# Optimization experiments

Hardware: AMD Instinct MI355X
Metric: run time of the kernel (lower is better)

The kernel has to match this reference:

```python
import jax, jax.numpy as jnp
import numpy as np

B, S, C = 16, 1024, 8
V, D, E, H, R = 50257, 512, 8, 512, 32
F, RT, CD, Q = 1024, 512, 64, 128
EPS = 1e-6


def _normalize(x):
    n = jnp.maximum(jnp.linalg.norm(x, axis=-1, keepdims=True), EPS)
    return x / n


def _fake_quantize(x):
    # F.normalize then straight-through int8 quant on the unit vector
    xn = _normalize(x)
    q = jnp.clip(jnp.round(xn * 127.0), -127.0, 127.0)
    return xn + jax.lax.stop_gradient(q / 127.0 - xn)


def setup_inputs() -> dict:
    key = jax.random.key(0)
    ks = iter(jax.random.split(key, 64))

    def w(shape, s=0.02):
        return (jax.random.normal(next(ks), shape, dtype=jnp.float32) * s)

    inp = {}
    inp['prefix_tokens'] = jax.random.randint(next(ks), (B, S), 0, V, dtype=jnp.int32)
    inp['chunk_inputs'] = jax.random.randint(next(ks), (B, C), 0, V, dtype=jnp.int32)
    inp['chunk_targets'] = jax.random.randint(next(ks), (B, C), 0, V, dtype=jnp.int32)
    inp['next_chunk_tokens'] = jax.random.randint(next(ks), (B, C), 0, V, dtype=jnp.int32)

    inp['emb'] = w((V, D))
    # stacked per-expert AffineExpert params
    inp['Wa'] = w((E, D, H)); inp['ba'] = jnp.zeros((E, H), jnp.float32)
    inp['Wg'] = w((E, D, R)); inp['bg'] = jnp.zeros((E, R), jnp.float32)
    inp['Wu'] = w((E, D, H)); inp['bu'] = jnp.zeros((E, H), jnp.float32)
    inp['u_mat'] = w((E, H, R)); inp['v_mat'] = w((E, H, R))
    inp['Wp'] = w((E, H, F)); inp['bp'] = jnp.zeros((E, F), jnp.float32)
    # gate MLP
    inp['Wg1'] = w((D, D)); inp['bg1'] = jnp.zeros((D,), jnp.float32)
    inp['Wg2'] = w((D, E)); inp['bg2'] = jnp.zeros((E,), jnp.float32)
    # query / target / key / code-expansion / write-code
    inp['Wq'] = w((F, Q)); inp['bq'] = jnp.zeros((Q,), jnp.float32)
    inp['Wt1'] = w((2 * D, RT)); inp['bt1'] = jnp.zeros((RT,), jnp.float32)
    inp['Wt2'] = w((RT, RT)); inp['bt2'] = jnp.zeros((RT,), jnp.float32)
    inp['Wk'] = w((RT, Q)); inp['bk'] = jnp.zeros((Q,), jnp.float32)
    inp['Web'] = w((CD, RT))  # expansion_basis (no bias)
    inp['Wwc'] = w((F, CD)); inp['bwc'] = jnp.zeros((CD,), jnp.float32)
    # ctx MLP
    inp['Wc1'] = w((2 * F, F)); inp['bc1'] = jnp.zeros((F,), jnp.float32)
    inp['Wc2'] = w((F, F)); inp['bc2'] = jnp.zeros((F,), jnp.float32)
    # chunk decoder
    inp['chunk_pos'] = w((C, F))
    inp['Wci'] = w((D + F, F)); inp['bci'] = jnp.zeros((F,), jnp.float32)
    inp['Wm1'] = w((F, F)); inp['bm1'] = jnp.zeros((F,), jnp.float32)
    inp['Wm2'] = w((F, F)); inp['bm2'] = jnp.zeros((F,), jnp.float32)
    inp['Wlm'] = w((F, V)); inp['blm'] = jnp.zeros((V,), jnp.float32)
    return inp


def _expert_scan(x, Wa, ba, Wg, bg, Wu, bu, u_mat, v_mat):
    # x: [B,S,D]; precompute all per-step projections as one big GEMM each,
    # leading axis = time for lax.scan. A,U: [S,E,B,H], G: [S,E,B,R]
    A = jax.nn.sigmoid(jnp.einsum('bsd,edh->sebh', x, Wa) + ba[None, :, None, :])
    G = jnp.einsum('bsd,edr->sebr', x, Wg) + bg[None, :, None, :]
    U = jnp.einsum('bsd,edh->sebh', x, Wu) + bu[None, :, None, :]

    def step(state, inp):  # state: [E,B,H]
        a, g, u = inp
        low = jnp.einsum('ebh,ehr->ebr', state, v_mat) * g
        state = a * state + u + jnp.einsum('ebr,ehr->ebh', low, u_mat)
        return state, None

    state0 = jnp.zeros((E, B, H), x.dtype)
    state, _ = jax.lax.scan(step, state0, (A, G, U))
    return state  # [E,B,H]


def reference(prefix_tokens, chunk_inputs, chunk_targets, next_chunk_tokens,
              emb, Wa, ba, Wg, bg, Wu, bu, u_mat, v_mat, Wp, bp,
              Wg1, bg1, Wg2, bg2, Wq, bq, Wt1, bt1, Wt2, bt2, Wk, bk,
              Web, Wwc, bwc, Wc1, bc1, Wc2, bc2,
              chunk_pos, Wci, bci, Wm1, bm1, Wm2, bm2, Wlm, blm):
    # ---- encode_prefix ----
    prefix_emb = emb[prefix_tokens]                       # [B,S,D]
    summary = prefix_emb.mean(axis=1)                     # [B,D]
    gate_probs = jax.nn.softmax(jax.nn.silu(summary @ Wg1 + bg1) @ Wg2 + bg2, axis=-1)  # [B,E]
    states = _expert_scan(prefix_emb, Wa, ba, Wg, bg, Wu, bu, u_mat, v_mat)             # [E,B,H]
    proj = jnp.einsum('ebh,ehf->ebf', states, Wp) + bp[:, None, :]                       # [E,B,F]
    fused = jnp.einsum('ebf,be->bf', proj, gate_probs)    # [B,F]

    # ---- query / target / key ----
    q_st = _fake_quantize(fused @ Wq + bq)                # [B,Q]
    chunk_emb = emb[chunk_targets].mean(axis=1)           # [B,D]
    next_emb = emb[next_chunk_tokens].mean(axis=1)        # [B,D]
    t_in = jnp.concatenate([chunk_emb, next_emb], axis=-1)
    target_state = _normalize(jax.nn.silu(t_in @ Wt1 + bt1) @ Wt2 + bt2)  # [B,RT]
    target_k_st = _fake_quantize(target_state @ Wk + bk)  # [B,Q]

    # ---- read_context (bank=None path -> zero read) ----
    zero_read = jnp.zeros_like(fused)
    c_in = jnp.concatenate([fused, zero_read], axis=-1)
    ctx = jax.nn.silu(c_in @ Wc1 + bc1) @ Wc2 + bc2       # [B,F]

    # ---- write_from_ctx ----
    write_codes = ctx @ Wwc + bwc                         # [B,CD]
    write_state = _normalize(write_codes @ Web)           # [B,RT]
    write_k_st = _fake_quantize(write_state @ Wk + bk)    # [B,Q]

    # ---- decode_chunk ----
    tok = emb[chunk_inputs]                               # [B,C,D]
    ctx_rep = jnp.broadcast_to(ctx[:, None, :], (B, C, F))
    hidden = jnp.concatenate([tok, ctx_rep], axis=-1) @ Wci + bci + chunk_pos[None]  # [B,C,F]
    hidden = jax.nn.silu(hidden @ Wm1 + bm1) @ Wm2 + bm2
    logits = hidden @ Wlm + blm                           # [B,C,V]

    # ---- losses ----
    logp = jax.nn.log_softmax(logits, axis=-1)
    token_loss = -jnp.take_along_axis(logp, chunk_targets[..., None], axis=-1)[..., 0]
    loss_nll = token_loss.mean()
    sim = (q_st @ target_k_st.T) / jnp.sqrt(jnp.float32(Q))  # [B,B]
    return logits, loss_nll, sim, write_k_st
```

## Files before the change

kernel.cpp:

```cpp
#include <hip/hip_runtime.h>
#include <math.h>

constexpr int BB = 16;
constexpr int SS = 1024;
constexpr int CC = 8;
constexpr int VV = 50257;
constexpr int DD = 512;
constexpr int EE = 8;
constexpr int HH = 512;
constexpr int RR = 32;
constexpr int FF = 1024;
constexpr int RTd = 512;
constexpr int CDd = 64;
constexpr int QQ = 128;
constexpr int SCH = 128;

typedef short bf16x8 __attribute__((ext_vector_type(8)));
typedef float f32x4 __attribute__((ext_vector_type(4)));

__device__ __forceinline__ float sigm(float x){ return 1.0f/(1.0f+expf(-x)); }

__device__ __forceinline__ unsigned short f2bf(float f){
  unsigned int u = __float_as_uint(f);
  u += 0x7fff + ((u>>16)&1);
  return (unsigned short)(u>>16);
}
__device__ __forceinline__ float bf2f(unsigned short h){
  return __uint_as_float(((unsigned int)h)<<16);
}

__device__ __forceinline__ void gload16(unsigned short* l, const unsigned short* g){
  __builtin_amdgcn_global_load_lds(
      (const __attribute__((address_space(1))) unsigned int*)(g),
      (__attribute__((address_space(3))) unsigned int*)(l), 16, 0, 0);
}

__global__ __launch_bounds__(256) void gather_pack(const int* __restrict__ toks,
    const float* __restrict__ emb, unsigned short* __restrict__ xp){
  int id = blockIdx.x*256 + threadIdx.x;
  int b = id >> 17;
  int rem = id & 131071;
  int c = rem >> 14;
  int rem2 = rem & 16383;
  int kc = rem2 >> 10;
  int pb = rem2 & 1023;
  int row = pb >> 3, q = pb & 7;
  int v = q ^ (row & 7);
  int kq = v >> 1, h = v & 1;
  int tok = toks[b*SS + c*128 + row];
  const float* src = emb + (size_t)tok*DD + kc*32 + kq*8;
  unsigned short o[8];
  #pragma unroll
  for (int j=0;j<8;j++){
    float f = src[j];
    unsigned short hi = f2bf(f);
    o[j] = h ? f2bf(f - bf2f(hi)) : hi;
  }
  ushort4* dst = (ushort4*)(xp + (size_t)id*8);
  dst[0] = make_ushort4(o[0],o[1],o[2],o[3]);
  dst[1] = make_ushort4(o[4],o[5],o[6],o[7]);
}

__global__ __launch_bounds__(512) void colsum_part(const int* __restrict__ toks,
    const float* __restrict__ emb, float* __restrict__ part){
  int b = blockIdx.y, j = blockIdx.x, d = threadIdx.x;
  float s = 0.f;
  for (int k=0;k<64;k++){
    int tok = toks[b*SS + j*64 + k];
    s += emb[(size_t)tok*DD + d];
  }
  part[(b*16 + j)*DD + d] = s;
}
__global__ __launch_bounds__(512) void colsum_final(const float* __restrict__ part,
                                                    float* __restrict__ summary){
  int b = blockIdx.x, d = threadIdx.x;
  float s = 0.f;
  for (int j=0;j<16;j++) s += part[(b*16 + j)*DD + d];
  summary[b*DD + d] = s * (1.0f/1024.0f);
}

__global__ __launch_bounds__(128) void gate_h1(const float* __restrict__ summary,
                                               const float* __restrict__ Wg1,
                                               const float* __restrict__ bg1,
                                               float* __restrict__ h1){
  int t = threadIdx.x; int j = blockIdx.x*128 + t;
  __shared__ float sm[16*512];
  for (int idx=t; idx<8192; idx+=128) sm[idx] = summary[idx];
  __syncthreads();
  float acc[16] = {0};
  for (int d=0; d<DD; d++){
    float w = Wg1[d*DD + j];
    #pragma unroll
    for (int b2=0;b2<16;b2++) acc[b2] += sm[b2*DD + d]*w;
  }
  #pragma unroll
  for (int b2=0;b2<16;b2++){ float v = acc[b2] + bg1[j]; h1[b2*DD + j] = v*sigm(v); }
}
__global__ __launch_bounds__(128) void gate_probs_k(const float* __restrict__ h1,
                                                    const float* __restrict__ Wg2,
                                                    const float* __restrict__ bg2,
                                                    float* __restrict__ gate){
  int t = threadIdx.x;
  int b = t>>3, e = t&7;
  float acc = bg2[e];
  for (int d=0; d<DD; d++) acc += h1[b*DD + d]*Wg2[d*EE + e];
  __shared__ float lg[16][8];
  lg[b][e] = acc;
  __syncthreads();
  if (e==0){
    float m = -3.4e38f;
    for (int i=0;i<8;i++) m = fmaxf(m, lg[b][i]);
    float s = 0.f; float ex[8];
    for (int i=0;i<8;i++){ ex[i] = expf(lg[b][i]-m); s += ex[i]; }
    for (int i=0;i<8;i++) gate[b*EE + i] = ex[i]/s;
  }
}

__global__ __launch_bounds__(256) void convT_pack_au(const float* __restrict__ Wa,
    const float* __restrict__ Wu, unsigned short* __restrict__ WPackAU){
  const int ec = blockIdx.x;
  const int kc = blockIdx.y;
  const int e = ec >> 3, ct = ec & 7;
  __shared__ float ta[32][64];
  __shared__ float tu[32][64];
  const int t = threadIdx.x;
  for (int i=0;i<8;i++){
    int id = t + i*256;
    int c = id & 63, kk = id >> 6;
    size_t src = ((size_t)e*DD + kc*32 + kk)*HH + ct*64 + c;
    ta[kk][c] = Wa[src];
    tu[kk][c] = Wu[src];
  }
  __syncthreads();
  unsigned short* o = WPackAU + ((size_t)ec*16 + kc)*8192;
  for (int i=0;i<8;i++){
    int idx4 = t + i*256;
    int blk = idx4 >> 1, half = idx4 & 1;
    int a = blk >> 8, kq = (blk >> 6) & 3, c = blk & 63;
    const float* src = (a >> 1) ? &tu[0][0] : &ta[0][0];
    unsigned short s4[4];
    #pragma unroll
    for (int j2=0;j2<4;j2++){
      int j = half*4 + j2;
      float f = src[(kq*8 + j)*64 + c];
      unsigned short hi = f2bf(f);
      s4[j2] = (a & 1) ? f2bf(f - bf2f(hi)) : hi;
    }
    *(ushort4*)&o[(size_t)idx4*4] = make_ushort4(s4[0],s4[1],s4[2],s4[3]);
  }
}
__global__ __launch_bounds__(256) void convT_pack_g(const float* __restrict__ Wge,
    unsigned short* __restrict__ WPackG){
  const int gt = blockIdx.x;
  const int kc = blockIdx.y;
  __shared__ float tg[32][64];
  const int t = threadIdx.x;
  for (int i=0;i<8;i++){
    int id = t + i*256;
    int c = id & 63, kk = id >> 6;
    int gcol = gt*64 + c;
    tg[kk][c] = Wge[((size_t)(gcol>>5)*DD + kc*32 + kk)*RR + (gcol & 31)];
  }
  __syncthreads();
  unsigned short* o = WPackG + ((size_t)gt*16 + kc)*4096;
  for (int i=0;i<4;i++){
    int idx4 = t + i*256;
    int blk = idx4 >> 1, half = idx4 & 1;
    int a = blk >> 8, kq = (blk >> 6) & 3, c = blk & 63;
    unsigned short s4[4];
    #pragma unroll
    for (int j2=0;j2<4;j2++){
      int j = half*4 + j2;
      float f = tg[kq*8 + j][c];
      unsigned short hi = f2bf(f);
      s4[j2] = a ? f2bf(f - bf2f(hi)) : hi;
    }
    *(ushort4*)&o[(size_t)idx4*4] = make_ushort4(s4[0],s4[1],s4[2],s4[3]);
  }
}

__global__ __launch_bounds__(512, 2) void aug_scan(
    const unsigned short* __restrict__ xp,
    const unsigned short* __restrict__ WPackAU, const unsigned short* __restrict__ WPackG,
    const float* __restrict__ ba, const float* __restrict__ bu, const float* __restrict__ bge,
    float* __restrict__ Aw, float* __restrict__ Uw, float* __restrict__ Gw,
    const float* __restrict__ Ar, const float* __restrict__ Ur, const float* __restrict__ Gr,
    const float* __restrict__ v_mat, const float* __restrict__ u_mat,
    float* __restrict__ states,
    int s0, int do_aug, int do_scan)
{
  __shared__ __align__(16) unsigned short lds[32768];
  const int t = threadIdx.x;

  if (blockIdx.x < 128){
    if (!do_scan) return;
    const int e = blockIdx.x >> 4;
    const int b = blockIdx.x & 15;
    const int r = t & 31, grp = t >> 5;
    float* stf   = (float*)lds;
    float* partf = (float*)lds + 1024;
    float* lowf  = (float*)lds + 1312;
    float vreg[32];
    #pragma unroll
    for (int i=0;i<32;i++) vreg[i] = v_mat[((size_t)e*HH + grp*32 + i)*RR + r];
    float ureg[32];
    {
      const float4* up = (const float4*)(u_mat + ((size_t)e*HH + t)*RR);
      #pragma unroll
      for (int j=0;j<8;j++){
        float4 v4 = up[j];
        ureg[j*4+0]=v4.x; ureg[j*4+1]=v4.y; ureg[j*4+2]=v4.z; ureg[j*4+3]=v4.w;
      }
    }
    const size_t base  = ((size_t)e*BB + b)*HH + t;
    const size_t gbase = ((size_t)e*BB + b)*RR + r;
    const size_t strAU = (size_t)EE*BB*HH;
    const size_t strG  = (size_t)EE*BB*RR;
    float streg = states[base];
    stf[t] = streg;
    float a0 = Ar[base], u0 = Ur[base];
    float g0 = (t < 32) ? Gr[gbase] : 0.f;
    float a1 = Ar[base + strAU], u1 = Ur[base + strAU];
    float g1 = (t < 32) ? Gr[gbase + strG] : 0.f;
    __syncthreads();
    int cur = 0;
    for (int s=0; s<SCH; s++){
      float a2 = 0.f, u2 = 0.f, g2 = 0.f;
      if (s+2 < SCH){
        a2 = Ar[base + (size_t)(s+2)*strAU];
        u2 = Ur[base + (size_t)(s+2)*strAU];
        if (t < 32) g2 = Gr[gbase + (size_t)(s+2)*strG];
      }
      float p = 0.f;
      #pragma unroll
      for (int i=0;i<32;i++) p += stf[cur*512 + grp*32+i]*vreg[i];
      p += __shfl_xor(p, 32, 64);
      if ((t & 32) == 0) partf[r*9 + (grp>>1)] = p;
      __syncthreads();
      if (t < 32){
        float ss2 = 0.f;
        #pragma unroll
        for (int j=0;j<8;j++) ss2 += partf[t*9 + j];
        lowf[t] = ss2 * g0;
      }
      __syncthreads();
      float acc2 = 0.f;
      #pragma unroll
      for (int i=0;i<32;i++) acc2 += lowf[i]*ureg[i];
      streg = a0*streg + u0 + acc2;
      stf[(cur^1)*512 + t] = streg;
      cur ^= 1;
      a0=a1; u0=u1; g0=g1; a1=a2; u1=u2; g1=g2;
      __syncthreads();
    }
    states[base] = streg;
    return;
  }

  if (!do_aug) return;
  const int aid = blockIdx.x - 128;
  const int b  = aid & 15;
  const int ct = aid >> 4;
  const int lane = t & 63, wv = t >> 6;
  const int cix = s0 >> 7;
  const unsigned short* xpc = xp + (((size_t)(b*8 + cix)) << 17);
  const int wo = wv*64;

  f32x4 acc[2][4] = {};
  const int cl15 = lane & 15;

  if (ct < 64){
    const int e = ct >> 3;
    const int c0 = (ct & 7)*64;
    const unsigned short* wpc = WPackAU + (((size_t)ct) << 17);
    const int strip = wv & 3;
    const int mode  = wv >> 2;
    const int kq4 = lane >> 4;
    const int rr0 = strip*32 + cl15, rr1 = rr0 + 16;
    const int qh = (kq4*2) ^ (rr0 & 7);
    const int ql = (kq4*2+1) ^ (rr0 & 7);
    const int ab = mode*512;

#define STAGE_AU(BUF, KC) { \
    unsigned short* XB_ = lds + (BUF)*16384; \
    unsigned short* WB_ = XB_ + 8192; \
    const unsigned short* gx = xpc + (KC)*8192; \
    const unsigned short* gw = wpc + (KC)*8192; \
    gload16(XB_ + wo*8,        gx + (size_t)(wo + lane)*8); \
    gload16(XB_ + (512+wo)*8,  gx + (size_t)(512 + wo + lane)*8); \
    gload16(WB_ + wo*8,        gw + (size_t)(wo + lane)*8); \
    gload16(WB_ + (512+wo)*8,  gw + (size_t)(512 + wo + lane)*8); }

    STAGE_AU(0, 0)
    asm volatile("s_waitcnt vmcnt(0)" ::: "memory");
    __builtin_amdgcn_s_barrier();
    __builtin_amdgcn_sched_barrier(0);
    int cur = 0;
    for (int kc=0; kc<16; kc++){
      if (kc < 15) STAGE_AU(cur^1, kc+1)
      const unsigned short* XB = lds + cur*16384;
      const unsigned short* WB = XB + 8192;
      bf16x8 ah0 = *(const bf16x8*)&XB[(rr0*8 + qh)*8];
      bf16x8 al0 = *(const bf16x8*)&XB[(rr0*8 + ql)*8];
      bf16x8 ah1 = *(const bf16x8*)&XB[(rr1*8 + qh)*8];
      bf16x8 al1 = *(const bf16x8*)&XB[(rr1*8 + ql)*8];
      #pragma unroll
      for (int cf=0; cf<4; cf++){
        const int cc = cf*16 + cl15;
        bf16x8 bh = *(const bf16x8*)&WB[(ab + kq4*64 + cc)*8];
        bf16x8 bl = *(const bf16x8*)&WB[(ab + 256 + kq4*64 + cc)*8];
        acc[0][cf] = __builtin_amdgcn_mfma_f32_16x16x32_bf16(ah0, bh, acc[0][cf], 0,0,0);
        acc[0][cf] = __builtin_amdgcn_mfma_f32_16x16x32_bf16(ah0, bl, acc[0][cf], 0,0,0);
        acc[0][cf] = __builtin_amdgcn_mfma_f32_16x16x32_bf16(al0, bh, acc[0][cf], 0,0,0);
        acc[1][cf] = __builtin_amdgcn_mfma_f32_16x16x32_bf16(ah1, bh, acc[1][cf], 0,0,0);
        acc[1][cf] = __builtin_amdgcn_mfma_f32_16x16x32_bf16(ah1, bl, acc[1][cf], 0,0,0);
        acc[1][cf] = __builtin_amdgcn_mfma_f32_16x16x32_bf16(al1, bh, acc[1][cf], 0,0,0);
      }
      __builtin_amdgcn_sched_barrier(0);
      asm volatile("s_waitcnt vmcnt(0)" ::: "memory");
      __builtin_amdgcn_s_barrier();
      __builtin_amdgcn_sched_barrier(0);
      cur ^= 1;
    }
#undef STAGE_AU
    const int r4 = (lane >> 4) * 4;
    #pragma unroll
    for (int rf=0; rf<2; rf++){
      #pragma unroll
      for (int cf=0; cf<4; cf++){
        #pragma unroll
        for (int i=0;i<4;i++){
          int sl = strip*32 + rf*16 + r4 + i;
          int ce = c0 + cf*16 + cl15;
          float v = acc[rf][cf][i];
          if (mode == 0){
            v += ba[e*HH + ce];
            v = sigm(v);
            Aw[((size_t)(sl*EE + e)*BB + b)*HH + ce] = v;
          } else {
            v += bu[e*HH + ce];
            Uw[((size_t)(sl*EE + e)*BB + b)*HH + ce] = v;
          }
        }
      }
    }
  } else {
    const int gt = ct - 64;
    const int c0 = gt*64;
    const unsigned short* wpc = WPackG + (((size_t)gt) << 16);
    const int kq4 = lane >> 4;
    const int rr0 = wv*16 + cl15;
    const int qh = (kq4*2) ^ (rr0 & 7);
    const int ql = (kq4*2+1) ^ (rr0 & 7);

#define STAGE_G(BUF, KC) { \
    unsigned short* XB_ = lds + (BUF)*16384; \
    unsigned short* WB_ = XB_ + 8192; \
    const unsigned short* gx = xpc + (KC)*8192; \
    const unsigned short* gw = wpc + (KC)*4096; \
    gload16(XB_ + wo*8,        gx + (size_t)(wo + lane)*8); \
    gload16(XB_ + (512+wo)*8,  gx + (size_t)(512 + wo + lane)*8); \
    gload16(WB_ + wo*8,        gw + (size_t)(wo + lane)*8); }

    STAGE_G(0, 0)
    asm volatile("s_waitcnt vmcnt(0)" ::: "memory");
    __builtin_amdgcn_s_barrier();
    __builtin_amdgcn_sched_barrier(0);
    int cur = 0;
    for (int kc=0; kc<16; kc++){
      if (kc < 15) STAGE_G(cur^1, kc+1)
      const unsigned short* XB = lds + cur*16384;
      const unsigned short* WB = XB + 8192;
      bf16x8 ah0 = *(const bf16x8*)&XB[(rr0*8 + qh)*8];
      bf16x8 al0 = *(const bf16x8*)&XB[(rr0*8 + ql)*8];
      #pragma unroll
      for (int cf=0; cf<4; cf++){
        const int cc = cf*16 + cl15;
        bf16x8 bh = *(const bf16x8*)&WB[(kq4*64 + cc)*8];
        bf16x8 bl = *(const bf16x8*)&WB[(256 + kq4*64 + cc)*8];
        acc[0][cf] = __builtin_amdgcn_mfma_f32_16x16x32_bf16(ah0, bh, acc[0][cf], 0,0,0);
        acc[0][cf] = __builtin_amdgcn_mfma_f32_16x16x32_bf16(ah0, bl, acc[0][cf], 0,0,0);
        acc[0][cf] = __builtin_amdgcn_mfma_f32_16x16x32_bf16(al0, bh, acc[0][cf], 0,0,0);
      }
      __builtin_amdgcn_sched_barrier(0);
      asm volatile("s_waitcnt vmcnt(0)" ::: "memory");
      __builtin_amdgcn_s_barrier();
      __builtin_amdgcn_sched_barrier(0);
      cur ^= 1;
    }
#undef STAGE_G
    const int r4 = (lane >> 4) * 4;
    #pragma unroll
    for (int cf=0; cf<4; cf++){
      #pragma unroll
      for (int i=0;i<4;i++){
        int sl = wv*16 + r4 + i;
        int g = c0 + cf*16 + cl15;
        int ee = g >> 5, r2 = g & 31;
        float v = acc[0][cf][i] + bge[ee*RR + r2];
        Gw[((size_t)(sl*EE + ee)*BB + b)*RR + r2] = v;
      }
    }
  }
}

__global__ __launch_bounds__(128) void proj_partial(const float* __restrict__ states,
    const float* __restrict__ Wp, const float* __restrict__ gate, float* __restrict__ pf){
  int fc = blockIdx.x, e = blockIdx.y, t = threadIdx.x;
  __shared__ float stl[16*512];
  for (int idx=t; idx<8192; idx+=128) stl[idx] = states[(size_t)e*8192 + idx];
  __syncthreads();
  int f = fc*128 + t;
  float acc[16] = {0};
  for (int h=0; h<HH; h++){
    float w = Wp[((size_t)e*HH + h)*FF + f];
    #pragma unroll
    for (int b2=0;b2<16;b2++) acc[b2] += stl[b2*HH + h]*w;
  }
  #pragma unroll
  for (int b2=0;b2<16;b2++) pf[((size_t)(e*16 + b2))*FF + f] = gate[b2*EE + e]*acc[b2];
}
__global__ __launch_bounds__(256) void fuse_reduce(const float* __restrict__ pf,
    const float* __restrict__ gate, const float* __restrict__ bp, float* __restrict__ fused){
  int idx = blockIdx.x*256 + threadIdx.x;
  int b = idx >> 10, f = idx & 1023;
  float s = 0.f;
  #pragma unroll
  for (int e=0;e<8;e++) s += pf[((size_t)(e*16 + b))*FF + f] + gate[b*EE + e]*bp[e*FF + f];
  fused[idx] = s;
}

__global__ __launch_bounds__(128) void fq_linear(const float* __restrict__ in, int Kin,
    const float* __restrict__ W, const float* __restrict__ bias, float* __restrict__ out){
  int b = blockIdx.x, t = threadIdx.x;
  __shared__ float xin[1024];
  __shared__ float red[2];
  for (int k=t;k<Kin;k+=128) xin[k] = in[(size_t)b*Kin + k];
  __syncthreads();
  float acc = bias[t];
  for (int k=0;k<Kin;k++) acc += xin[k]*W[k*QQ + t];
  float ss = acc*acc;
  #pragma unroll
  for (int off=32; off; off>>=1) ss += __shfl_xor(ss, off, 64);
  if ((t&63)==0) red[t>>6] = ss;
  __syncthreads();
  float n = fmaxf(sqrtf(red[0]+red[1]), 1e-6f);
  float xn = acc / n;
  float q = fminf(fmaxf(rintf(xn*127.0f), -127.0f), 127.0f) * (1.0f/127.0f);
  out[b*QQ + t] = q;
}

__global__ __launch_bounds__(512) void chunk_means(const int* __restrict__ ct,
    const int* __restrict__ nct, const float* __restrict__ emb, float* __restrict__ tin){
  int b = blockIdx.x, d = threadIdx.x;
  float ce=0.f, ne=0.f;
  for (int c=0;c<CC;c++){
    ce += emb[(size_t)ct[b*CC+c]*DD + d];
    ne += emb[(size_t)nct[b*CC+c]*DD + d];
  }
  tin[b*1024 + d] = ce*0.125f;
  tin[b*1024 + 512 + d] = ne*0.125f;
}

__global__ __launch_bounds__(512) void target_state_kernel(const float* __restrict__ tin,
    const float* __restrict__ Wt1, const float* __restrict__ bt1,
    const float* __restrict__ Wt2, const float* __restrict__ bt2, float* __restrict__ outts){
  int b = blockIdx.x, t = threadIdx.x;
  __shared__ float xin[1024];
  __shared__ float h1[512];
  __shared__ float red[8];
  for (int k=t;k<1024;k+=512) xin[k] = tin[b*1024 + k];
  __syncthreads();
  float acc = bt1[t];
  for (int k=0;k<1024;k++) acc += xin[k]*Wt1[k*RTd + t];
  acc = acc*sigm(acc);
  h1[t] = acc;
  __syncthreads();
  float y = bt2[t];
  for (int k=0;k<512;k++) y += h1[k]*Wt2[k*RTd + t];
  float ss = y*y;
  #pragma unroll
  for (int off=32; off; off>>=1) ss += __shfl_xor(ss, off, 64);
  if ((t&63)==0) red[t>>6] = ss;
  __syncthreads();
  float tot = 0.f;
  #pragma unroll
  for (int i=0;i<8;i++) tot += red[i];
  float n = fmaxf(sqrtf(tot), 1e-6f);
  outts[b*RTd + t] = y/n;
}

__global__ __launch_bounds__(512) void write_state_kernel(const float* __restrict__ ctx,
    const float* __restrict__ Wwc, const float* __restrict__ bwc,
    const float* __restrict__ Web, float* __restrict__ wsn){
  int b = blockIdx.x, t = threadIdx.x;
  __shared__ float cx[1024];
  __shared__ float wc[64];
  __shared__ float red[8];
  for (int k=t;k<1024;k+=512) cx[k] = ctx[b*FF + k];
  __syncthreads();
  if (t < 64){
    float a = bwc[t];
    for (int k=0;k<1024;k++) a += cx[k]*Wwc[k*CDd + t];
    wc[t] = a;
  }
  __syncthreads();
  float y = 0.f;
  for (int k=0;k<64;k++) y += wc[k]*Web[k*RTd + t];
  float ss = y*y;
  #pragma unroll
  for (int off=32; off; off>>=1) ss += __shfl_xor(ss, off, 64);
  if ((t&63)==0) red[t>>6] = ss;
  __syncthreads();
  float tot = 0.f;
  #pragma unroll
  for (int i=0;i<8;i++) tot += red[i];
  float n = fmaxf(sqrtf(tot), 1e-6f);
  wsn[b*RTd + t] = y/n;
}

__global__ __launch_bounds__(256) void sim_kernel(const float* __restrict__ q,
    const float* __restrict__ k, float* __restrict__ out){
  int t = threadIdx.x;
  int i = t>>4, j = t&15;
  float s = 0.f;
  for (int c=0;c<QQ;c++) s += q[i*QQ + c]*k[j*QQ + c];
  out[t] = s / sqrtf(128.0f);
}

__global__ __launch_bounds__(256) void build_xcat(const int* __restrict__ ci,
    const float* __restrict__ emb, const float* __restrict__ ctx, float* __restrict__ xcat){
  int idx = blockIdx.x*256 + threadIdx.x;
  int row = idx / 1536, k = idx % 1536;
  float v = (k < DD) ? emb[(size_t)ci[row]*DD + k] : ctx[(row>>3)*FF + (k - DD)];
  xcat[idx] = v;
}

__global__ __launch_bounds__(256) void gemm_part(const float* __restrict__ X,
    const float* __restrict__ W, float* __restrict__ part,
    int K, int KS, int M){
  const int t = threadIdx.x;
  const int col = blockIdx.x*64 + (t & 63);
  const int r0 = blockIdx.y*16;
  const int ks = blockIdx.z;
  const int rg = t >> 6;
  const int kslice = K / KS;
  const int kbeg = ks*kslice;
  __shared__ float xs[16][65];
  float acc[4] = {};
  for (int k0=kbeg; k0<kbeg+kslice; k0+=64){
    #pragma unroll
    for (int i=0;i<4;i++){
      int id = t + i*256;
      int row = id >> 6, kk = id & 63;
      xs[row][kk] = X[(size_t)(r0+row)*K + k0 + kk];
    }
    __syncthreads();
    #pragma unroll 8
    for (int kk=0; kk<64; kk++){
      float w = W[(size_t)(k0+kk)*FF + col];
      #pragma unroll
      for (int i=0;i<4;i++) acc[i] += xs[rg*4+i][kk]*w;
    }
    __syncthreads();
  }
  #pragma unroll
  for (int i=0;i<4;i++)
    part[((size_t)ks*M + r0 + rg*4 + i)*FF + col] = acc[i];
}
__global__ __launch_bounds__(256) void gemm_combine(const float* __restrict__ part,
    const float* __restrict__ bias, const float* __restrict__ pos,
    float* __restrict__ outp, int KS, int M, int act){
  int idx = blockIdx.x*256 + threadIdx.x;
  int row = idx >> 10, col = idx & 1023;
  float v = bias[col];
  for (int k=0;k<KS;k++) v += part[(size_t)k*M*FF + idx];
  if (pos) v += pos[(row & 7)*FF + col];
  if (act) v = v*sigm(v);
  outp[idx] = v;
}

__global__ __launch_bounds__(256) void split_h(const float* __restrict__ hsrc,
    unsigned short* __restrict__ hh, unsigned short* __restrict__ hl){
  int idx = blockIdx.x*256 + threadIdx.x;
  float f = hsrc[idx];
  unsigned short h = f2bf(f);
  hh[idx] = h;
  hl[idx] = f2bf(f - bf2f(h));
}

__global__ __launch_bounds__(256) void logits_mfma(
    const unsigned short* __restrict__ hh, const unsigned short* __restrict__ hl,
    const float* __restrict__ Wlm, const float* __restrict__ blm,
    float* __restrict__ out){
  const int t = threadIdx.x;
  const int lane = t & 63, w = t >> 6;
  const int cb = blockIdx.x * 64;
  __shared__ __align__(16) unsigned short xsh[8*128*8];
  __shared__ __align__(16) unsigned short xsl[8*128*8];
  __shared__ __align__(16) unsigned short wsh[8*64*8];
  __shared__ __align__(16) unsigned short wsl[8*64*8];
  f32x4 acc[2][4] = {};
  for (int kc=0; kc<16; kc++){
    const int k0 = kc*64;
    #pragma unroll
    for (int i=0;i<4;i++){
      int id = t + i*256;
      int kq = id & 7, row = id >> 3;
      int pb = row*8 + (kq ^ (row&7));
      *(uint4*)&xsh[pb*8] = *(const uint4*)(hh + (size_t)row*FF + k0 + kq*8);
      *(uint4*)&xsl[pb*8] = *(const uint4*)(hl + (size_t)row*FF + k0 + kq*8);
    }
    #pragma unroll
    for (int i=0;i<2;i++){
      int id = t + i*256;
      int cc = id & 63, kq = id >> 6;
      int c = cb + cc; if (c >= VV) c = VV - 1;
      unsigned short h8[8], l8[8];
      #pragma unroll
      for (int j=0;j<8;j++){
        float f = Wlm[(size_t)(k0 + kq*8 + j)*VV + c];
        unsigned short h = f2bf(f);
        h8[j] = h;
        l8[j] = f2bf(f - bf2f(h));
      }
      int pb = kq*64 + cc;
      *(ushort4*)&wsh[pb*8]   = make_ushort4(h8[0],h8[1],h8[2],h8[3]);
      *(ushort4*)&wsh[pb*8+4] = make_ushort4(h8[4],h8[5],h8[6],h8[7]);
      *(ushort4*)&wsl[pb*8]   = make_ushort4(l8[0],l8[1],l8[2],l8[3]);
      *(ushort4*)&wsl[pb*8+4] = make_ushort4(l8[4],l8[5],l8[6],l8[7]);
    }
    __syncthreads();
    #pragma unroll
    for (int ks=0; ks<2; ks++){
      const int kq4 = ks*4 + (lane>>4);
      const int rr0 = w*32 + (lane&15);
      const int rr1 = rr0 + 16;
      bf16x8 ah0 = *(const bf16x8*)&xsh[(rr0*8 + (kq4^(rr0&7)))*8];
      bf16x8 ah1 = *(const bf16x8*)&xsh[(rr1*8 + (kq4^(rr1&7)))*8];
      bf16x8 al0 = *(const bf16x8*)&xsl[(rr0*8 + (kq4^(rr0&7)))*8];
      bf16x8 al1 = *(const bf16x8*)&xsl[(rr1*8 + (kq4^(rr1&7)))*8];
      #pragma unroll
      for (int cf=0; cf<4; cf++){
        const int cc = cf*16 + (lane&15);
        bf16x8 bh = *(const bf16x8*)&wsh[(kq4*64 + cc)*8];
        bf16x8 bl = *(const bf16x8*)&wsl[(kq4*64 + cc)*8];
        acc[0][cf] = __builtin_amdgcn_mfma_f32_16x16x32_bf16(ah0, bh, acc[0][cf], 0,0,0);
        acc[0][cf] = __builtin_amdgcn_mfma_f32_16x16x32_bf16(ah0, bl, acc[0][cf], 0,0,0);
        acc[0][cf] = __builtin_amdgcn_mfma_f32_16x16x32_bf16(al0, bh, acc[0][cf], 0,0,0);
        acc[1][cf] = __builtin_amdgcn_mfma_f32_16x16x32_bf16(ah1, bh, acc[1][cf], 0,0,0);
        acc[1][cf] = __builtin_amdgcn_mfma_f32_16x16x32_bf16(ah1, bl, acc[1][cf], 0,0,0);
        acc[1][cf] = __builtin_amdgcn_mfma_f32_16x16x32_bf16(al1, bh, acc[1][cf], 0,0,0);
      }
    }
    __syncthreads();
  }
  const int cl = lane & 15;
  const int r4 = (lane >> 4) * 4;
  #pragma unroll
  for (int rf=0; rf<2; rf++){
    #pragma unroll
    for (int cf=0; cf<4; cf++){
      int c = cb + cf*16 + cl;
      if (c >= VV) continue;
      float bb = blm[c];
      #pragma unroll
      for (int i=0;i<4;i++){
        int row = w*32 + rf*16 + r4 + i;
        out[(size_t)row*VV + c] = acc[rf][cf][i] + bb;
      }
    }
  }
}

__global__ __launch_bounds__(512) void softmax_nll(const float* __restrict__ logits,
    const int* __restrict__ tgt, float* __restrict__ tl){
  const int row = blockIdx.x;
  const float* p = logits + (size_t)row*VV;
  const int t = threadIdx.x;
  float m = -3.4e38f, s = 0.f;
  for (int c=t; c<VV; c+=512){
    float v = p[c];
    if (v > m){ s = s*expf(m - v) + 1.0f; m = v; }
    else s += expf(v - m);
  }
  #pragma unroll
  for (int off=32; off; off>>=1){
    float m2 = __shfl_xor(m, off, 64);
    float s2 = __shfl_xor(s, off, 64);
    float mn = fmaxf(m, m2);
    s = s*expf(m - mn) + s2*expf(m2 - mn);
    m = mn;
  }
  __shared__ float ms[8], ssh[8];
  if ((t&63)==0){ ms[t>>6] = m; ssh[t>>6] = s; }
  __syncthreads();
  if (t==0){
    float M = ms[0], S = ssh[0];
    for (int i=1;i<8;i++){
      float mn = fmaxf(M, ms[i]);
      S = S*expf(M-mn) + ssh[i]*expf(ms[i]-mn);
      M = mn;
    }
    tl[row] = M + logf(S) - p[tgt[row]];
  }
}
__global__ __launch_bounds__(128) void loss_reduce(const float* __restrict__ tl,
                                                   float* __restrict__ out){
  int t = threadIdx.x;
  float v = tl[t];
  #pragma unroll
  for (int off=32; off; off>>=1) v += __shfl_xor(v, off, 64);
  __shared__ float r2[2];
  if ((t&63)==0) r2[t>>6] = v;
  __syncthreads();
  if (t==0) out[0] = (r2[0]+r2[1]) * (1.0f/128.0f);
}

extern "C" void kernel_launch(void* const* d_in, const int* in_sizes, int n_in,
                              void* d_out, int out_size, void* d_ws, size_t ws_size,
                              hipStream_t stream){
  (void)in_sizes; (void)n_in; (void)out_size;
  const int*  prefix = (const int*)d_in[0];
  const int*  cinp   = (const int*)d_in[1];
  const int*  ctgt   = (const int*)d_in[2];
  const int*  nctk   = (const int*)d_in[3];
  const float* emb  = (const float*)d_in[4];
  const float* Wa   = (const float*)d_in[5];
  const float* ba   = (const float*)d_in[6];
  const float* Wge  = (const float*)d_in[7];
  const float* bge  = (const float*)d_in[8];
  const float* Wu   = (const float*)d_in[9];
  const float* bu   = (const float*)d_in[10];
  const float* u_mat= (const float*)d_in[11];
  const float* v_mat= (const float*)d_in[12];
  const float* Wp   = (const float*)d_in[13];
  const float* bp   = (const float*)d_in[14];
  const float* Wg1  = (const float*)d_in[15];
  const float* bg1  = (const float*)d_in[16];
  const float* Wg2  = (const float*)d_in[17];
  const float* bg2  = (const float*)d_in[18];
  const float* Wq   = (const float*)d_in[19];
  const float* bq   = (const float*)d_in[20];
  const float* Wt1  = (const float*)d_in[21];
  const float* bt1  = (const float*)d_in[22];
  const float* Wt2  = (const float*)d_in[23];
  const float* bt2  = (const float*)d_in[24];
  const float* Wk   = (const float*)d_in[25];
  const float* bk   = (const float*)d_in[26];
  const float* Web  = (const float*)d_in[27];
  const float* Wwc  = (const float*)d_in[28];
  const float* bwc  = (const float*)d_in[29];
  const float* Wc1  = (const float*)d_in[30];
  const float* bc1  = (const float*)d_in[31];
  const float* Wc2  = (const float*)d_in[32];
  const float* bc2  = (const float*)d_in[33];
  const float* cpos = (const float*)d_in[34];
  const float* Wci  = (const float*)d_in[35];
  const float* bci  = (const float*)d_in[36];
  const float* Wm1  = (const float*)d_in[37];
  const float* bm1  = (const float*)d_in[38];
  const float* Wm2  = (const float*)d_in[39];
  const float* bm2  = (const float*)d_in[40];
  const float* Wlm  = (const float*)d_in[41];
  const float* blm  = (const float*)d_in[42];

  float* ws = (float*)d_ws;
  size_t off = 0;
  unsigned short* xp = (unsigned short*)(ws + off); off += (size_t)BB*SS*DD;
  float* Abuf0  = ws + off; off += (size_t)SCH*EE*BB*HH;
  float* Ubuf0  = ws + off; off += (size_t)SCH*EE*BB*HH;
  float* Gbuf0  = ws + off; off += (size_t)SCH*EE*BB*RR;
  float* statesb= ws + off; off += (size_t)EE*BB*HH;
  float* partb  = ws + off; off += (size_t)BB*16*DD;
  float* summb  = ws + off; off += (size_t)BB*DD;
  float* h1b    = ws + off; off += (size_t)BB*DD;
  float* gateb  = ws + off; off += (size_t)BB*EE;
  float* pfb    = ws + off; off += (size_t)EE*BB*FF;
  float* fusedb = ws + off; off += (size_t)BB*FF;
  float* qstb   = ws + off; off += (size_t)BB*QQ;
  float* tinb   = ws + off; off += (size_t)BB*2*DD;
  float* tstb   = ws + off; off += (size_t)BB*RTd;
  float* tkb    = ws + off; off += (size_t)BB*QQ;
  float* ctxb   = ws + off; off += (size_t)BB*FF;
  float* hctxb  = ws + off; off += (size_t)BB*FF;
  float* wsnb   = ws + off; off += (size_t)BB*RTd;
  float* xcatb  = ws + off; off += (size_t)BB*CC*(DD+FF);
  float* hid1b  = ws + off; off += (size_t)BB*CC*FF;
  float* h2b    = ws + off; off += (size_t)BB*CC*FF;
  float* hidb   = ws + off; off += (size_t)BB*CC*FF;
  float* tlb    = ws + off; off += (size_t)BB*CC;
  float* ppart  = ws + off; off += (size_t)4*BB*CC*FF;
  unsigned short* WPackAU = (unsigned short*)(ws + off); off += (size_t)EE*DD*HH*2;
  unsigned short* WPackG  = (unsigned short*)(ws + off); off += (size_t)EE*DD*RR;
  unsigned short* hhb  = (unsigned short*)(ws + off); off += (size_t)BB*CC*FF/2;
  unsigned short* hlb  = (unsigned short*)(ws + off); off += (size_t)BB*CC*FF/2;
  float* Abuf1  = ws + off; off += (size_t)SCH*EE*BB*HH;
  float* Ubuf1  = ws + off; off += (size_t)SCH*EE*BB*HH;
  float* Gbuf1  = ws + off; off += (size_t)SCH*EE*BB*RR;
  const bool fused = ws_size >= off * sizeof(float);

  float* out = (float*)d_out;
  const size_t LOGITS_OFF = 0;
  const size_t LOSS_OFF = (size_t)BB*CC*VV;
  const size_t SIM_OFF  = LOSS_OFF + 1;
  const size_t WK_OFF   = SIM_OFF + (size_t)BB*BB;

  convT_pack_au<<<dim3(64,16), 256, 0, stream>>>(Wa, Wu, WPackAU);
  convT_pack_g<<<dim3(4,16), 256, 0, stream>>>(Wge, WPackG);

  gather_pack<<<8192, 256, 0, stream>>>(prefix, emb, xp);
  colsum_part<<<dim3(16,16), 512, 0, stream>>>(prefix, emb, partb);
  colsum_final<<<16, 512, 0, stream>>>(partb, summb);
  gate_h1<<<4, 128, 0, stream>>>(summb, Wg1, bg1, h1b);
  gate_probs_k<<<1, 128, 0, stream>>>(h1b, Wg2, bg2, gateb);

  hipMemsetAsync(statesb, 0, (size_t)EE*BB*HH*sizeof(float), stream);

  if (fused){
    for (int c=0; c<=8; c++){
      int da = (c<8) ? 1 : 0;
      int dscn = (c>=1) ? 1 : 0;
      float* Aw = (c&1) ? Abuf1 : Abuf0;
      float* Uw = (c&1) ? Ubuf1 : Ubuf0;
      float* Gw = (c&1) ? Gbuf1 : Gbuf0;
      const float* Ar = ((c-1)&1) ? Abuf1 : Abuf0;
      const float* Ur = ((c-1)&1) ? Ubuf1 : Ubuf0;
      const float* Gr = ((c-1)&1) ? Gbuf1 : Gbuf0;
      int grid = da ? 1216 : 128;
      aug_scan<<<grid, 512, 0, stream>>>(xp, WPackAU, WPackG, ba, bu, bge,
          Aw, Uw, Gw, Ar, Ur, Gr, v_mat, u_mat, statesb,
          c*SCH, da, dscn);
    }
  } else {
    for (int c=0; c<8; c++){
      aug_scan<<<1216, 512, 0, stream>>>(xp, WPackAU, WPackG, ba, bu, bge,
          Abuf0, Ubuf0, Gbuf0, Abuf0, Ubuf0, Gbuf0, v_mat, u_mat, statesb,
          c*SCH, 1, 0);
      aug_scan<<<128, 512, 0, stream>>>(xp, WPackAU, WPackG, ba, bu, bge,
          Abuf0, Ubuf0, Gbuf0, Abuf0, Ubuf0, Gbuf0, v_mat, u_mat, statesb,
          c*SCH, 0, 1);
    }
  }

  proj_partial<<<dim3(8,8), 128, 0, stream>>>(statesb, Wp, gateb, pfb);
  fuse_reduce<<<64, 256, 0, stream>>>(pfb, gateb, bp, fusedb);

  fq_linear<<<16, 128, 0, stream>>>(fusedb, FF, Wq, bq, qstb);
  chunk_means<<<16, 512, 0, stream>>>(ctgt, nctk, emb, tinb);
  target_state_kernel<<<16, 512, 0, stream>>>(tinb, Wt1, bt1, Wt2, bt2, tstb);
  fq_linear<<<16, 128, 0, stream>>>(tstb, RTd, Wk, bk, tkb);

  gemm_part<<<dim3(16,1,4), 256, 0, stream>>>(fusedb, Wc1, ppart, FF, 4, 16);
  gemm_combine<<<64, 256, 0, stream>>>(ppart, bc1, nullptr, hctxb, 4, 16, 1);
  gemm_part<<<dim3(16,1,4), 256, 0, stream>>>(hctxb, Wc2, ppart, FF, 4, 16);
  gemm_combine<<<64, 256, 0, stream>>>(ppart, bc2, nullptr, ctxb, 4, 16, 0);

  write_state_kernel<<<16, 512, 0, stream>>>(ctxb, Wwc, bwc, Web, wsnb);
  fq_linear<<<16, 128, 0, stream>>>(wsnb, RTd, Wk, bk, out + WK_OFF);
  sim_kernel<<<1, 256, 0, stream>>>(qstb, tkb, out + SIM_OFF);

  build_xcat<<<768, 256, 0, stream>>>(cinp, emb, ctxb, xcatb);
  gemm_part<<<dim3(16,8,4), 256, 0, stream>>>(xcatb, Wci, ppart, DD+FF, 4, 128);
  gemm_combine<<<512, 256, 0, stream>>>(ppart, bci, cpos, hid1b, 4, 128, 0);
  gemm_part<<<dim3(16,8,4), 256, 0, stream>>>(hid1b, Wm1, ppart, FF, 4, 128);
  gemm_combine<<<512, 256, 0, stream>>>(ppart, bm1, nullptr, h2b, 4, 128, 1);
  gemm_part<<<dim3(16,8,4), 256, 0, stream>>>(h2b, Wm2, ppart, FF, 4, 128);
  gemm_combine<<<512, 256, 0, stream>>>(ppart, bm2, nullptr, hidb, 4, 128, 0);

  split_h<<<512, 256, 0, stream>>>(hidb, hhb, hlb);
  logits_mfma<<<(VV+63)/64, 256, 0, stream>>>(hhb, hlb, Wlm, blm, out + LOGITS_OFF);

  softmax_nll<<<BB*CC, 512, 0, stream>>>(out + LOGITS_OFF, ctgt, tlb);
  loss_reduce<<<1, 128, 0, stream>>>(tlb, out + LOSS_OFF);
}
```

Before: 1.611 ms.

## Precompute V^T U to cut one barrier per step in the recurrent scan

A new kernel precomputes the per-expert 32x32 matrix V^T U. The scan loop splits the next step's low-rank projection into the part from a*st+u, computed as a full block reduction, and a V^T U correction applied to the current low vector by 32 threads. This lets the per-step chain run with two barriers instead of three, shortening the serial critical path of the 128-block scan. The cost is extra small arithmetic, a prologue step, more shared memory, and a different floating-point summation order.

```diff
diff --git a/kernel.cpp b/kernel.cpp
--- a/kernel.cpp
+++ b/kernel.cpp
@@ -61,6 +61,17 @@
   dst[1] = make_ushort4(o[4],o[5],o[6],o[7]);
 }
 
+__global__ __launch_bounds__(256) void compute_vu(const float* __restrict__ v_mat,
+    const float* __restrict__ u_mat, float* __restrict__ VU){
+  int e = blockIdx.x, qtr = blockIdx.y;
+  int pair = qtr*256 + threadIdx.x;
+  int r = pair >> 5, rp = pair & 31;
+  float acc = 0.f;
+  for (int h=0; h<HH; h++)
+    acc += v_mat[((size_t)e*HH + h)*RR + r] * u_mat[((size_t)e*HH + h)*RR + rp];
+  VU[e*1024 + pair] = acc;
+}
+
 __global__ __launch_bounds__(512) void colsum_part(const int* __restrict__ toks,
     const float* __restrict__ emb, float* __restrict__ part){
   int b = blockIdx.y, j = blockIdx.x, d = threadIdx.x;
@@ -186,6 +197,7 @@
     float* __restrict__ Aw, float* __restrict__ Uw, float* __restrict__ Gw,
     const float* __restrict__ Ar, const float* __restrict__ Ur, const float* __restrict__ Gr,
     const float* __restrict__ v_mat, const float* __restrict__ u_mat,
+    const float* __restrict__ VU,
     float* __restrict__ states,
     int s0, int do_aug, int do_scan)
 {
@@ -197,9 +209,11 @@
     const int e = blockIdx.x >> 4;
     const int b = blockIdx.x & 15;
     const int r = t & 31, grp = t >> 5;
-    float* stf   = (float*)lds;
-    float* partf = (float*)lds + 1024;
-    float* lowf  = (float*)lds + 1312;
+    float* F     = (float*)lds;
+    float* lowf  = F;
+    float* partf = F + 64;
+    float* ybuf  = F + 64 + 576;
+    float* vuf   = F + 64 + 576 + 512;
     float vreg[32];
     #pragma unroll
     for (int i=0;i<32;i++) vreg[i] = v_mat[((size_t)e*HH + grp*32 + i)*RR + r];
@@ -212,18 +226,57 @@
         ureg[j*4+0]=v4.x; ureg[j*4+1]=v4.y; ureg[j*4+2]=v4.z; ureg[j*4+3]=v4.w;
       }
     }
+    for (int i=t; i<1024; i+=512) vuf[(i>>5)*33 + (i&31)] = VU[e*1024 + i];
     const size_t base  = ((size_t)e*BB + b)*HH + t;
-    const size_t gbase = ((size_t)e*BB + b)*RR + r;
+    const size_t gbase = ((size_t)e*BB + b)*RR + (t & 31);
     const size_t strAU = (size_t)EE*BB*HH;
     const size_t strG  = (size_t)EE*BB*RR;
-    float streg = states[base];
-    stf[t] = streg;
+    float st = states[base];
     float a0 = Ar[base], u0 = Ur[base];
-    float g0 = (t < 32) ? Gr[gbase] : 0.f;
     float a1 = Ar[base + strAU], u1 = Ur[base + strAU];
-    float g1 = (t < 32) ? Gr[gbase + strG] : 0.f;
+    float g0reg = (t < 32) ? Gr[gbase] : 0.f;
+    float g1reg = (t < 32) ? Gr[gbase + strG] : 0.f;
+    ybuf[t] = st;
     __syncthreads();
-    int cur = 0;
+    {
+      const float* yb = &ybuf[grp*32];
+      float p0=0,p1=0,p2=0,p3=0;
+      #pragma unroll
+      for (int i=0;i<8;i++){
+        p0 += yb[i]*vreg[i];       p1 += yb[8+i]*vreg[8+i];
+        p2 += yb[16+i]*vreg[16+i]; p3 += yb[24+i]*vreg[24+i];
+      }
+      float p = (p0+p1)+(p2+p3);
+      p += __shfl_xor(p, 32, 64);
+      if ((t & 32) == 0) partf[288 + r*9 + (grp>>1)] = p;
+    }
+    __syncthreads();
+    if (t < 32){
+      float z0 = 0.f;
+      #pragma unroll
+      for (int j=0;j<8;j++) z0 += partf[288 + t*9 + j];
+      lowf[t] = z0 * g0reg;
+    }
+    {
+      float y0 = a0*st + u0;
+      __syncthreads();
+      ybuf[t] = y0;
+    }
+    __syncthreads();
+    {
+      const float* yb = &ybuf[grp*32];
+      float p0=0,p1=0,p2=0,p3=0;
+      #pragma unroll
+      for (int i=0;i<8;i++){
+        p0 += yb[i]*vreg[i];       p1 += yb[8+i]*vreg[8+i];
+        p2 += yb[16+i]*vreg[16+i]; p3 += yb[24+i]*vreg[24+i];
+      }
+      float p = (p0+p1)+(p2+p3);
+      p += __shfl_xor(p, 32, 64);
+      if ((t & 32) == 0) partf[r*9 + (grp>>1)] = p;
+    }
+    __syncthreads();
+    int par = 0;
     for (int s=0; s<SCH; s++){
       float a2 = 0.f, u2 = 0.f, g2 = 0.f;
       if (s+2 < SCH){
@@ -231,29 +284,52 @@
         u2 = Ur[base + (size_t)(s+2)*strAU];
         if (t < 32) g2 = Gr[gbase + (size_t)(s+2)*strG];
       }
-      float p = 0.f;
-      #pragma unroll
-      for (int i=0;i<32;i++) p += stf[cur*512 + grp*32+i]*vreg[i];
-      p += __shfl_xor(p, 32, 64);
-      if ((t & 32) == 0) partf[r*9 + (grp>>1)] = p;
+      {
+        const float* lw = &lowf[par*32];
+        float q0=0,q1=0,q2=0,q3=0;
+        #pragma unroll
+        for (int i=0;i<8;i++){
+          q0 += lw[i]*ureg[i];       q1 += lw[8+i]*ureg[8+i];
+          q2 += lw[16+i]*ureg[16+i]; q3 += lw[24+i]*ureg[24+i];
+        }
+        st = a0*st + u0 + ((q0+q1)+(q2+q3));
+      }
+      float yv = a1*st + u1;
+      ybuf[t] = yv;
       __syncthreads();
-      if (t < 32){
-        float ss2 = 0.f;
+      {
+        const float* yb = &ybuf[grp*32];
+        float p0=0,p1=0,p2=0,p3=0;
         #pragma unroll
-        for (int j=0;j<8;j++) ss2 += partf[t*9 + j];
-        lowf[t] = ss2 * g0;
+        for (int i=0;i<8;i++){
+          p0 += yb[i]*vreg[i];       p1 += yb[8+i]*vreg[8+i];
+          p2 += yb[16+i]*vreg[16+i]; p3 += yb[24+i]*vreg[24+i];
+        }
+        float p = (p0+p1)+(p2+p3);
+        p += __shfl_xor(p, 32, 64);
+        if ((t & 32) == 0) partf[(par^1)*288 + r*9 + (grp>>1)] = p;
+      }
+      if (t < 32 && s < SCH-1){
+        float z = 0.f;
+        #pragma unroll
+        for (int j=0;j<8;j++) z += partf[par*288 + t*9 + j];
+        const float* lw = &lowf[par*32];
+        const float* vr = &vuf[t*33];
+        float z0=0,z1=0,z2=0,z3=0;
+        #pragma unroll
+        for (int i=0;i<8;i++){
+          z0 += vr[i]*lw[i];       z1 += vr[8+i]*lw[8+i];
+          z2 += vr[16+i]*lw[16+i]; z3 += vr[24+i]*lw[24+i];
+        }
+        z += (z0+z1)+(z2+z3);
+        lowf[(par^1)*32 + t] = z * g1reg;
       }
       __syncthreads();
-      float acc2 = 0.f;
-      #pragma unroll
-      for (int i=0;i<32;i++) acc2 += lowf[i]*ureg[i];
-      streg = a0*streg + u0 + acc2;
-      stf[(cur^1)*512 + t] = streg;
-      cur ^= 1;
-      a0=a1; u0=u1; g0=g1; a1=a2; u1=u2; g1=g2;
-      __syncthreads();
-    }
-    states[base] = streg;
+      a0=a1; u0=u1; a1=a2; u1=u2;
+      g0reg=g1reg; g1reg=g2;
+      par ^= 1;
+    }
+    states[base] = st;
     return;
   }
 
@@ -795,6 +871,7 @@
   unsigned short* WPackG  = (unsigned short*)(ws + off); off += (size_t)EE*DD*RR;
   unsigned short* hhb  = (unsigned short*)(ws + off); off += (size_t)BB*CC*FF/2;
   unsigned short* hlb  = (unsigned short*)(ws + off); off += (size_t)BB*CC*FF/2;
+  float* vub    = ws + off; off += (size_t)EE*RR*RR;
   float* Abuf1  = ws + off; off += (size_t)SCH*EE*BB*HH;
   float* Ubuf1  = ws + off; off += (size_t)SCH*EE*BB*HH;
   float* Gbuf1  = ws + off; off += (size_t)SCH*EE*BB*RR;
@@ -808,6 +885,7 @@
 
   convT_pack_au<<<dim3(64,16), 256, 0, stream>>>(Wa, Wu, WPackAU);
   convT_pack_g<<<dim3(4,16), 256, 0, stream>>>(Wge, WPackG);
+  compute_vu<<<dim3(8,4), 256, 0, stream>>>(v_mat, u_mat, vub);
 
   gather_pack<<<8192, 256, 0, stream>>>(prefix, emb, xp);
   colsum_part<<<dim3(16,16), 512, 0, stream>>>(prefix, emb, partb);
@@ -829,16 +907,16 @@
       const float* Gr = ((c-1)&1) ? Gbuf1 : Gbuf0;
       int grid = da ? 1216 : 128;
       aug_scan<<<grid, 512, 0, stream>>>(xp, WPackAU, WPackG, ba, bu, bge,
-          Aw, Uw, Gw, Ar, Ur, Gr, v_mat, u_mat, statesb,
+          Aw, Uw, Gw, Ar, Ur, Gr, v_mat, u_mat, vub, statesb,
           c*SCH, da, dscn);
     }
   } else {
     for (int c=0; c<8; c++){
       aug_scan<<<1216, 512, 0, stream>>>(xp, WPackAU, WPackG, ba, bu, bge,
-          Abuf0, Ubuf0, Gbuf0, Abuf0, Ubuf0, Gbuf0, v_mat, u_mat, statesb,
+          Abuf0, Ubuf0, Gbuf0, Abuf0, Ubuf0, Gbuf0, v_mat, u_mat, vub, statesb,
           c*SCH, 1, 0);
       aug_scan<<<128, 512, 0, stream>>>(xp, WPackAU, WPackG, ba, bu, bge,
-          Abuf0, Ubuf0, Gbuf0, Abuf0, Ubuf0, Gbuf0, v_mat, u_mat, statesb,
+          Abuf0, Ubuf0, Gbuf0, Abuf0, Ubuf0, Gbuf0, v_mat, u_mat, vub, statesb,
           c*SCH, 0, 1);
     }
   }
```

Measured after the change: 1.867 ms. 1.16x slower.
